# Optimization experiments

Measured on AMD Instinct MI355X. Metric: run time of the kernel, lower is better.

## Reference

```python
import jax, jax.numpy as jnp
import numpy as np

B, T, D, H, W = 256, 512, 64, 128, 256

def _init_linear(key, out_dim, in_dim):
    lim = 1.0 / np.sqrt(in_dim)
    return jax.random.uniform(key, (out_dim, in_dim), jnp.float32, -lim, lim)

def setup_inputs():
    key = jax.random.key(0)
    ks = jax.random.split(key, 12)
    inp = {}
    inp['ts'] = jnp.arange(T, dtype=jnp.float32)
    for n, k in zip(['coeffs_d', 'coeffs_c', 'coeffs_b', 'coeffs_a'], ks[:4]):
        inp[n] = jax.random.normal(k, (B, T - 1, D), jnp.float32) * 0.05
    # initial MLP: D -> W -> W -> H (relu hidden, identity final)
    inp['i_w0'] = _init_linear(ks[4], W, D); inp['i_b0'] = jnp.zeros((W,), jnp.float32)
    inp['i_w1'] = _init_linear(ks[5], W, W); inp['i_b1'] = jnp.zeros((W,), jnp.float32)
    inp['i_w2'] = _init_linear(ks[6], H, W); inp['i_b2'] = jnp.zeros((H,), jnp.float32)
    # func MLP: H -> W -> W -> H*D (softplus hidden, tanh final)
    inp['f_w0'] = _init_linear(ks[7], W, H); inp['f_b0'] = jnp.zeros((W,), jnp.float32)
    inp['f_w1'] = _init_linear(ks[8], W, W); inp['f_b1'] = jnp.zeros((W,), jnp.float32)
    inp['f_w2'] = _init_linear(ks[9], H * D, W); inp['f_b2'] = jnp.zeros((H * D,), jnp.float32)
    # readout linear: H -> 1
    inp['l_w'] = _init_linear(ks[10], 1, H); inp['l_b'] = jnp.zeros((1,), jnp.float32)
    return inp

def reference(ts, coeffs_d, coeffs_c, coeffs_b, coeffs_a,
              i_w0, i_b0, i_w1, i_b1, i_w2, i_b2,
              f_w0, f_b0, f_w1, f_b1, f_w2, f_b2,
              l_w, l_b):
    dt = ts[1] - ts[0]
    # cubic spline value at t=ts[0]: interval 0, frac 0 -> a[0]
    x0 = coeffs_a[:, 0, :]  # [B, D]
    h = jax.nn.relu(x0 @ i_w0.T + i_b0)
    h = jax.nn.relu(h @ i_w1.T + i_b1)
    y0 = h @ i_w2.T + i_b2  # [B, H]

    def step(carry, _):
        t, y = carry
        # cubic spline derivative at t: b + 2c*frac + 3d*frac^2 on interval idx
        idx = jnp.clip(jnp.searchsorted(ts, t, side='right') - 1, 0, T - 2)
        frac = t - ts[idx]
        deriv = coeffs_b[:, idx] + 2.0 * coeffs_c[:, idx] * frac + 3.0 * coeffs_d[:, idx] * (frac * frac)  # [B, D]
        # vector field f(y): [B, H, D]
        g = jax.nn.softplus(y @ f_w0.T + f_b0)
        g = jax.nn.softplus(g @ f_w1.T + f_b1)
        f = jnp.tanh(g @ f_w2.T + f_b2).reshape(B, H, D)
        # Euler step: y1 = y + (f @ dX/dt) * dt
        y1 = y + jnp.einsum('bhd,bd->bh', f, deriv) * dt
        return (t + dt, y1), y1

    _, ys = jax.lax.scan(step, (ts[0], y0), None, length=T)
    # prediction = sigmoid(linear(ys[-1]))[0], per batch element
    return jax.nn.sigmoid(ys[-1] @ l_w.T + l_b)[:, 0]  # [B]
```

## Files before the change

### kernel.cpp

```cpp
#include <hip/hip_runtime.h>
#include <hip/hip_bf16.h>
#include <stdint.h>


#define BB 256
#define DD 64
#define HH 128
#define WW 256
#define HD 8192
#define TSTEPS 512
#define PAD_Y 136
#define PAD_G 264

#define SM_W2   0
#define SM_YB   131072
#define SM_G    140288
#define SM_PBUF 157184
#define SM_TOT  158208

typedef __bf16 bf16x8 __attribute__((ext_vector_type(8)));
typedef __bf16 bf16x4 __attribute__((ext_vector_type(4)));
typedef float f32x4 __attribute__((ext_vector_type(4)));

__device__ __forceinline__ float softplus_f(float x) {
  return (x > 15.f) ? x : __logf(1.f + __expf(x));
}
__device__ __forceinline__ float tanh_f(float x) {
  float e = __expf(2.f * x);
  return 1.f - 2.f / (e + 1.f);
}
__device__ __forceinline__ void publish_y(uint32_t* slot, int idx, float val, uint32_t tag) {
  unsigned short ub = __builtin_bit_cast(unsigned short, (__bf16)val);
  __hip_atomic_store(&slot[idx], (tag << 16) | (uint32_t)ub,
                     __ATOMIC_RELAXED, __HIP_MEMORY_SCOPE_AGENT);
}

__global__ void prep_kernel(const float* __restrict__ w0, const float* __restrict__ w1,
                            const float* __restrict__ w2,
                            __bf16* __restrict__ w0b, __bf16* __restrict__ w1b,
                            __bf16* __restrict__ w2b) {
  int stride = gridDim.x * blockDim.x;
  int i0 = blockIdx.x * blockDim.x + threadIdx.x;
  for (int i = i0; i < WW * HH; i += stride) w0b[i] = (__bf16)w0[i];
  for (int i = i0; i < WW * WW; i += stride) w1b[i] = (__bf16)w1[i];
  for (int i = i0; i < HD * WW; i += stride) w2b[i] = (__bf16)w2[i];
}

__global__ __launch_bounds__(256) void init_kernel(
    const float* __restrict__ ca, const float* __restrict__ iw0, const float* __restrict__ ib0,
    const float* __restrict__ iw1, const float* __restrict__ ib1,
    const float* __restrict__ iw2, const float* __restrict__ ib2,
    float* __restrict__ y0) {
  __shared__ float x0[DD];
  __shared__ float h0[WW];
  __shared__ float h1[WW];
  int b = blockIdx.x, t = threadIdx.x;
  if (t < DD) x0[t] = ca[((size_t)b * 511) * DD + t];
  __syncthreads();
  float a = ib0[t];
  for (int d = 0; d < DD; ++d) a = fmaf(x0[d], iw0[t * DD + d], a);
  h0[t] = fmaxf(a, 0.f);
  __syncthreads();
  a = ib1[t];
  for (int d = 0; d < WW; ++d) a = fmaf(h0[d], iw1[t * WW + d], a);
  h1[t] = fmaxf(a, 0.f);
  __syncthreads();
  if (t < HH) {
    a = ib2[t];
    for (int d = 0; d < WW; ++d) a = fmaf(h1[d], iw2[t * WW + d], a);
    y0[b * HH + t] = a;
  }
}

__global__ __attribute__((amdgpu_flat_work_group_size(512, 512), amdgpu_waves_per_eu(2, 2)))
void step_persist(
    const __bf16* __restrict__ w0b, const __bf16* __restrict__ w1b, const __bf16* __restrict__ w2b,
    const float* __restrict__ fb0, const float* __restrict__ fb1, const float* __restrict__ fb2,
    const float* __restrict__ cbp, const float* __restrict__ ccp, const float* __restrict__ cdp,
    float* __restrict__ yA, uint32_t* __restrict__ pk)
{
  extern __shared__ __align__(16) char smem[];
  __bf16* w2l = (__bf16*)(smem + SM_W2);
  __bf16* yb  = (__bf16*)(smem + SM_YB);
  __bf16* g   = (__bf16*)(smem + SM_G);
  float* pbuf = (float*)(smem + SM_PBUF);

  const int tid = threadIdx.x;
  const int wv = tid >> 6;
  const int l = tid & 63;
  const int l16 = l & 15;
  const int lq = l >> 4;

  const int wid = blockIdx.x;
  const int grp = wid >> 5;
  const int j = wid & 31;
  const int rb = grp * 32;
  const int c0 = j * 256;

  for (int blk = tid; blk < 8192; blk += 512) {
    int kq = blk >> 8, col = blk & 255;
    int kb = kq >> 2, lq2 = kq & 3;
    *(bf16x8*)&w2l[(size_t)blk * 8] =
        *(const bf16x8*)&w2b[(size_t)(c0 + col) * WW + kb * 32 + lq2 * 8];
  }

  f32x4 b0r[2], b1r[2], b2r[2];
  #pragma unroll
  for (int c = 0; c < 2; ++c) {
    b0r[c] = *(const f32x4*)&fb0[wv * 32 + c * 16 + lq * 4];
    b1r[c] = *(const f32x4*)&fb1[wv * 32 + c * 16 + lq * 4];
    b2r[c] = *(const f32x4*)&fb2[c0 + wv * 32 + c * 16 + lq * 4];
  }

  size_t cb2[2];
  #pragma unroll
  for (int bt = 0; bt < 2; ++bt)
    cb2[bt] = ((size_t)(rb + bt * 16 + l16) * 511) * DD + (wv & 1) * 32 + lq * 4;

  const int w2base = lq * 2048 + (wv * 32 + l16) * 8;

  float yreg = 0.f;
  int myidx = 0;
  if (tid < 128) {
    int r = tid & 31, hl = tid >> 5;
    myidx = (rb + r) * HH + (4 * j + hl);
    yreg = yA[myidx];
    publish_y(pk, myidx, yreg, 1u);
  }
  __syncthreads();

  for (int k = 0; k < TSTEPS; ++k) {
    const uint32_t want = (uint32_t)(k + 1);
    const uint32_t* src = pk + (size_t)(k & 1) * (BB * HH);

    bf16x8 w0f[4][2], w1f[8][2];
    #pragma unroll
    for (int c = 0; c < 2; ++c) {
      int col = wv * 32 + c * 16 + l16;
      #pragma unroll
      for (int kb = 0; kb < 4; ++kb)
        w0f[kb][c] = *(const bf16x8*)&w0b[col * HH + kb * 32 + lq * 8];
      #pragma unroll
      for (int kb = 0; kb < 8; ++kb)
        w1f[kb][c] = *(const bf16x8*)&w1b[col * WW + kb * 32 + lq * 8];
    }
    __asm__ __volatile__("" ::: "memory");

    {
      uint32_t v[8];
      int ad[8];
      #pragma unroll
      for (int q = 0; q < 8; ++q) {
        int i = tid + q * 512;
        ad[q] = (rb + (i >> 7)) * HH + (i & (HH - 1));
        v[q] = __hip_atomic_load(&src[ad[q]], __ATOMIC_RELAXED, __HIP_MEMORY_SCOPE_AGENT);
      }
      int spins = 0;
      bool allok;
      do {
        allok = true;
        #pragma unroll
        for (int q = 0; q < 8; ++q) {
          if ((v[q] >> 16) != want) {
            allok = false;
            v[q] = __hip_atomic_load(&src[ad[q]], __ATOMIC_RELAXED, __HIP_MEMORY_SCOPE_AGENT);
          }
        }
        if (!allok) {
          __builtin_amdgcn_s_sleep(1);
          if (++spins > (1 << 20)) break;
        }
      } while (!allok);
      #pragma unroll
      for (int q = 0; q < 8; ++q) {
        int i = tid + q * 512;
        yb[(i >> 7) * PAD_Y + (i & (HH - 1))] =
            __builtin_bit_cast(__bf16, (unsigned short)(v[q] & 0xFFFFu));
      }
    }
    __syncthreads();

    {
      f32x4 acc[2][2] = {};
      #pragma unroll
      for (int kb = 0; kb < 4; ++kb) {
        bf16x8 y0 = *(const bf16x8*)&yb[l16 * PAD_Y + kb * 32 + lq * 8];
        bf16x8 y1 = *(const bf16x8*)&yb[(16 + l16) * PAD_Y + kb * 32 + lq * 8];
        #pragma unroll
        for (int c = 0; c < 2; ++c) {
          acc[c][0] = __builtin_amdgcn_mfma_f32_16x16x32_bf16(w0f[kb][c], y0, acc[c][0], 0, 0, 0);
          acc[c][1] = __builtin_amdgcn_mfma_f32_16x16x32_bf16(w0f[kb][c], y1, acc[c][1], 0, 0, 0);
        }
      }
      #pragma unroll
      for (int c = 0; c < 2; ++c)
        #pragma unroll
        for (int bt = 0; bt < 2; ++bt) {
          bf16x4 o;
          #pragma unroll
          for (int r = 0; r < 4; ++r)
            o[r] = (__bf16)softplus_f(acc[c][bt][r] + b0r[c][r]);
          *(bf16x4*)&g[(bt * 16 + l16) * PAD_G + wv * 32 + c * 16 + lq * 4] = o;
        }
    }
    __syncthreads();

    f32x4 dv_[2][2];
    {
      size_t ko = (size_t)((k <= 510) ? k : 510) * DD;
      #pragma unroll
      for (int bt = 0; bt < 2; ++bt)
        #pragma unroll
        for (int c = 0; c < 2; ++c) {
          size_t off = cb2[bt] + ko + c * 16;
          dv_[bt][c] = *(const f32x4*)&cbp[off];
          if (k == 511) {
            f32x4 cc = *(const f32x4*)&ccp[off];
            f32x4 dd = *(const f32x4*)&cdp[off];
            #pragma unroll
            for (int r = 0; r < 4; ++r)
              dv_[bt][c][r] += 2.f * cc[r] + 3.f * dd[r];
          }
        }
    }

    f32x4 acc1[2][2] = {};
    {
      #pragma unroll
      for (int kb = 0; kb < 8; ++kb) {
        bf16x8 a0 = *(const bf16x8*)&g[l16 * PAD_G + kb * 32 + lq * 8];
        bf16x8 a1 = *(const bf16x8*)&g[(16 + l16) * PAD_G + kb * 32 + lq * 8];
        #pragma unroll
        for (int c = 0; c < 2; ++c) {
          acc1[c][0] = __builtin_amdgcn_mfma_f32_16x16x32_bf16(w1f[kb][c], a0, acc1[c][0], 0, 0, 0);
          acc1[c][1] = __builtin_amdgcn_mfma_f32_16x16x32_bf16(w1f[kb][c], a1, acc1[c][1], 0, 0, 0);
        }
      }
    }
    __syncthreads();

    #pragma unroll
    for (int c = 0; c < 2; ++c)
      #pragma unroll
      for (int bt = 0; bt < 2; ++bt) {
        bf16x4 o;
        #pragma unroll
        for (int r = 0; r < 4; ++r)
          o[r] = (__bf16)softplus_f(acc1[c][bt][r] + b1r[c][r]);
        *(bf16x4*)&g[(bt * 16 + l16) * PAD_G + wv * 32 + c * 16 + lq * 4] = o;
      }
    __syncthreads();

    {
      f32x4 acc[2][2] = {};
      #pragma unroll
      for (int kb = 0; kb < 8; ++kb) {
        bf16x8 a0 = *(const bf16x8*)&g[l16 * PAD_G + kb * 32 + lq * 8];
        bf16x8 a1 = *(const bf16x8*)&g[(16 + l16) * PAD_G + kb * 32 + lq * 8];
        #pragma unroll
        for (int c = 0; c < 2; ++c) {
          bf16x8 wf = *(const bf16x8*)&w2l[w2base + kb * 8192 + c * 128];
          acc[c][0] = __builtin_amdgcn_mfma_f32_16x16x32_bf16(wf, a0, acc[c][0], 0, 0, 0);
          acc[c][1] = __builtin_amdgcn_mfma_f32_16x16x32_bf16(wf, a1, acc[c][1], 0, 0, 0);
        }
      }
      #pragma unroll
      for (int bt = 0; bt < 2; ++bt) {
        float p = 0.f;
        #pragma unroll
        for (int c = 0; c < 2; ++c) {
          #pragma unroll
          for (int r = 0; r < 4; ++r) {
            float f = tanh_f(acc[c][bt][r] + b2r[c][r]);
            p = fmaf(f, dv_[bt][c][r], p);
          }
        }
        p += __shfl_xor(p, 16);
        p += __shfl_xor(p, 32);
        if (l < 16) pbuf[wv * 32 + bt * 16 + l] = p;
      }
    }
    __syncthreads();

    if (tid < 128) {
      int hl = tid >> 5, r = tid & 31;
      yreg += pbuf[(2 * hl) * 32 + r] + pbuf[(2 * hl + 1) * 32 + r];
      publish_y(pk + (size_t)((k + 1) & 1) * (BB * HH), myidx, yreg, (uint32_t)(k + 2));
    }
    __syncthreads();
  }

  if (tid < 128) yA[myidx] = yreg;
}

__global__ __launch_bounds__(256) void final_kernel(const float* __restrict__ y,
                                                    const float* __restrict__ lw,
                                                    const float* __restrict__ lb,
                                                    float* __restrict__ out) {
  int b = threadIdx.x;
  float a = lb[0];
  for (int h = 0; h < HH; ++h) a = fmaf(y[b * HH + h], lw[h], a);
  out[b] = 1.f / (1.f + __expf(-a));
}

extern "C" void kernel_launch(void* const* d_in, const int* in_sizes, int n_in,
                              void* d_out, int out_size, void* d_ws, size_t ws_size,
                              hipStream_t stream) {
  const float* cdp = (const float*)d_in[1];
  const float* ccp = (const float*)d_in[2];
  const float* cbp = (const float*)d_in[3];
  const float* cap = (const float*)d_in[4];
  const float* iw0 = (const float*)d_in[5];
  const float* ib0 = (const float*)d_in[6];
  const float* iw1 = (const float*)d_in[7];
  const float* ib1 = (const float*)d_in[8];
  const float* iw2 = (const float*)d_in[9];
  const float* ib2 = (const float*)d_in[10];
  const float* fw0 = (const float*)d_in[11];
  const float* fb0 = (const float*)d_in[12];
  const float* fw1 = (const float*)d_in[13];
  const float* fb1 = (const float*)d_in[14];
  const float* fw2 = (const float*)d_in[15];
  const float* fb2 = (const float*)d_in[16];
  const float* lw  = (const float*)d_in[17];
  const float* lb  = (const float*)d_in[18];

  char* ws = (char*)d_ws;
  __bf16* w0b = (__bf16*)(ws);
  __bf16* w1b = (__bf16*)(ws + 65536);
  __bf16* w2b = (__bf16*)(ws + 65536 + 131072);
  float* yA = (float*)(ws + 65536 + 131072 + 4194304);
  uint32_t* pk = (uint32_t*)(ws + 65536 + 131072 + 4194304 + 131072);

  hipMemsetAsync(pk, 0, 2 * BB * HH * sizeof(uint32_t), stream);
  prep_kernel<<<512, 256, 0, stream>>>(fw0, fw1, fw2, w0b, w1b, w2b);
  init_kernel<<<BB, 256, 0, stream>>>(cap, iw0, ib0, iw1, ib1, iw2, ib2, yA);
  step_persist<<<256, 512, SM_TOT, stream>>>(w0b, w1b, w2b, fb0, fb1, fb2,
                                             cbp, ccp, cdp, yA, pk);
  final_kernel<<<1, 256, 0, stream>>>(yA, lw, lb, (float*)d_out);

  (void)in_sizes; (void)n_in; (void)out_size; (void)ws_size;
}
```

Baseline: 4.361 ms.

## Split each block's batch tile into two 16-row halves and publish per half

Each persistent block now handles its 32 batch rows as two 16-row sub-tiles, processed one after the other within each time step. Each half waits only for its own 16 rows of y and publishes them as soon as it finishes. The intent is to overlap the grid-wide spin-wait latency of one half with the compute of the other, and to give layer 1 and layer 2 separate shared-memory buffers so one barrier goes away. In exchange, the bf16 weight fragments are reloaded from global memory twice per step, each MFMA pass has half the batch width, and there are more barriers per step.

```diff
diff --git a/kernel.cpp b/kernel.cpp
--- a/kernel.cpp
+++ b/kernel.cpp
@@ -14,9 +14,10 @@
 
 #define SM_W2   0
 #define SM_YB   131072
-#define SM_G    140288
-#define SM_PBUF 157184
-#define SM_TOT  158208
+#define SM_G0   135424
+#define SM_G1   143872
+#define SM_PBUF 152320
+#define SM_TOT  152832
 
 typedef __bf16 bf16x8 __attribute__((ext_vector_type(8)));
 typedef __bf16 bf16x4 __attribute__((ext_vector_type(4)));
@@ -28,6 +29,9 @@
 __device__ __forceinline__ float tanh_f(float x) {
   float e = __expf(2.f * x);
   return 1.f - 2.f / (e + 1.f);
+}
+__device__ __forceinline__ uint32_t aload(const uint32_t* p) {
+  return __hip_atomic_load(p, __ATOMIC_RELAXED, __HIP_MEMORY_SCOPE_AGENT);
 }
 __device__ __forceinline__ void publish_y(uint32_t* slot, int idx, float val, uint32_t tag) {
   unsigned short ub = __builtin_bit_cast(unsigned short, (__bf16)val);
@@ -82,7 +86,8 @@
   extern __shared__ __align__(16) char smem[];
   __bf16* w2l = (__bf16*)(smem + SM_W2);
   __bf16* yb  = (__bf16*)(smem + SM_YB);
-  __bf16* g   = (__bf16*)(smem + SM_G);
+  __bf16* g0s = (__bf16*)(smem + SM_G0);
+  __bf16* g1s = (__bf16*)(smem + SM_G1);
   float* pbuf = (float*)(smem + SM_PBUF);
 
   const int tid = threadIdx.x;
@@ -92,9 +97,9 @@
   const int lq = l >> 4;
 
   const int wid = blockIdx.x;
-  const int grp = wid >> 5;
+  const int p = wid >> 5;
   const int j = wid & 31;
-  const int rb = grp * 32;
+  const int rb0 = p * 32;
   const int c0 = j * 256;
 
   for (int blk = tid; blk < 8192; blk += 512) {
@@ -103,6 +108,7 @@
     *(bf16x8*)&w2l[(size_t)blk * 8] =
         *(const bf16x8*)&w2b[(size_t)(c0 + col) * WW + kb * 32 + lq2 * 8];
   }
+  const int w2base = lq * 2048 + (wv * 32 + l16) * 8;
 
   f32x4 b0r[2], b1r[2], b2r[2];
   #pragma unroll
@@ -114,183 +120,172 @@
 
   size_t cb2[2];
   #pragma unroll
-  for (int bt = 0; bt < 2; ++bt)
-    cb2[bt] = ((size_t)(rb + bt * 16 + l16) * 511) * DD + (wv & 1) * 32 + lq * 4;
-
-  const int w2base = lq * 2048 + (wv * 32 + l16) * 8;
-
-  float yreg = 0.f;
-  int myidx = 0;
-  if (tid < 128) {
-    int r = tid & 31, hl = tid >> 5;
-    myidx = (rb + r) * HH + (4 * j + hl);
-    yreg = yA[myidx];
-    publish_y(pk, myidx, yreg, 1u);
+  for (int s = 0; s < 2; ++s)
+    cb2[s] = ((size_t)(rb0 + 16 * s + l16) * 511) * DD + (wv & 1) * 32 + lq * 4;
+
+  float yreg[2] = {0.f, 0.f};
+  int myidx[2] = {0, 0};
+  if (tid < 64) {
+    int r = tid & 15, hl = tid >> 4;
+    #pragma unroll
+    for (int s = 0; s < 2; ++s) {
+      myidx[s] = (rb0 + 16 * s + r) * HH + (4 * j + hl);
+      yreg[s] = yA[myidx[s]];
+      publish_y(pk, myidx[s], yreg[s], 1u);
+    }
   }
   __syncthreads();
 
   for (int k = 0; k < TSTEPS; ++k) {
     const uint32_t want = (uint32_t)(k + 1);
     const uint32_t* src = pk + (size_t)(k & 1) * (BB * HH);
-
-    bf16x8 w0f[4][2], w1f[8][2];
+    uint32_t* dst = pk + (size_t)((k + 1) & 1) * (BB * HH);
+
     #pragma unroll
-    for (int c = 0; c < 2; ++c) {
-      int col = wv * 32 + c * 16 + l16;
+    for (int s = 0; s < 2; ++s) {
+      const int rbs = rb0 + 16 * s;
+
+      bf16x8 w0f[4][2], w1f[8][2];
       #pragma unroll
-      for (int kb = 0; kb < 4; ++kb)
-        w0f[kb][c] = *(const bf16x8*)&w0b[col * HH + kb * 32 + lq * 8];
-      #pragma unroll
-      for (int kb = 0; kb < 8; ++kb)
-        w1f[kb][c] = *(const bf16x8*)&w1b[col * WW + kb * 32 + lq * 8];
-    }
-    __asm__ __volatile__("" ::: "memory");
-
-    {
-      uint32_t v[8];
-      int ad[8];
-      #pragma unroll
-      for (int q = 0; q < 8; ++q) {
-        int i = tid + q * 512;
-        ad[q] = (rb + (i >> 7)) * HH + (i & (HH - 1));
-        v[q] = __hip_atomic_load(&src[ad[q]], __ATOMIC_RELAXED, __HIP_MEMORY_SCOPE_AGENT);
-      }
-      int spins = 0;
-      bool allok;
-      do {
-        allok = true;
-        #pragma unroll
-        for (int q = 0; q < 8; ++q) {
-          if ((v[q] >> 16) != want) {
-            allok = false;
-            v[q] = __hip_atomic_load(&src[ad[q]], __ATOMIC_RELAXED, __HIP_MEMORY_SCOPE_AGENT);
-          }
-        }
-        if (!allok) {
-          __builtin_amdgcn_s_sleep(1);
-          if (++spins > (1 << 20)) break;
-        }
-      } while (!allok);
-      #pragma unroll
-      for (int q = 0; q < 8; ++q) {
-        int i = tid + q * 512;
-        yb[(i >> 7) * PAD_Y + (i & (HH - 1))] =
-            __builtin_bit_cast(__bf16, (unsigned short)(v[q] & 0xFFFFu));
-      }
-    }
-    __syncthreads();
-
-    {
-      f32x4 acc[2][2] = {};
-      #pragma unroll
-      for (int kb = 0; kb < 4; ++kb) {
-        bf16x8 y0 = *(const bf16x8*)&yb[l16 * PAD_Y + kb * 32 + lq * 8];
-        bf16x8 y1 = *(const bf16x8*)&yb[(16 + l16) * PAD_Y + kb * 32 + lq * 8];
+      for (int c = 0; c < 2; ++c) {
+        int col = wv * 32 + c * 16 + l16;
+        #pragma unroll
+        for (int kb = 0; kb < 4; ++kb)
+          w0f[kb][c] = *(const bf16x8*)&w0b[col * HH + kb * 32 + lq * 8];
+        #pragma unroll
+        for (int kb = 0; kb < 8; ++kb)
+          w1f[kb][c] = *(const bf16x8*)&w1b[col * WW + kb * 32 + lq * 8];
+      }
+      __asm__ __volatile__("" ::: "memory");
+
+      {
+        uint32_t v[4];
+        int ad[4];
+        #pragma unroll
+        for (int q = 0; q < 4; ++q) {
+          int i = tid + q * 512;
+          ad[q] = (rbs + (i >> 7)) * HH + (i & 127);
+          v[q] = aload(&src[ad[q]]);
+        }
+        int spins = 0;
+        bool allok;
+        do {
+          allok = true;
+          #pragma unroll
+          for (int q = 0; q < 4; ++q) {
+            if ((v[q] >> 16) != want) {
+              allok = false;
+              v[q] = aload(&src[ad[q]]);
+            }
+          }
+          if (!allok) {
+            __builtin_amdgcn_s_sleep(1);
+            if (++spins > (1 << 20)) break;
+          }
+        } while (!allok);
+        #pragma unroll
+        for (int q = 0; q < 4; ++q) {
+          int i = tid + q * 512;
+          yb[(i >> 7) * PAD_Y + (i & 127)] =
+              __builtin_bit_cast(__bf16, (unsigned short)(v[q] & 0xFFFFu));
+        }
+      }
+
+      f32x4 dvv[2];
+      {
+        size_t ko = (size_t)((k <= 510) ? k : 510) * DD;
         #pragma unroll
         for (int c = 0; c < 2; ++c) {
-          acc[c][0] = __builtin_amdgcn_mfma_f32_16x16x32_bf16(w0f[kb][c], y0, acc[c][0], 0, 0, 0);
-          acc[c][1] = __builtin_amdgcn_mfma_f32_16x16x32_bf16(w0f[kb][c], y1, acc[c][1], 0, 0, 0);
-        }
-      }
-      #pragma unroll
-      for (int c = 0; c < 2; ++c)
-        #pragma unroll
-        for (int bt = 0; bt < 2; ++bt) {
-          bf16x4 o;
-          #pragma unroll
-          for (int r = 0; r < 4; ++r)
-            o[r] = (__bf16)softplus_f(acc[c][bt][r] + b0r[c][r]);
-          *(bf16x4*)&g[(bt * 16 + l16) * PAD_G + wv * 32 + c * 16 + lq * 4] = o;
-        }
-    }
-    __syncthreads();
-
-    f32x4 dv_[2][2];
-    {
-      size_t ko = (size_t)((k <= 510) ? k : 510) * DD;
-      #pragma unroll
-      for (int bt = 0; bt < 2; ++bt)
-        #pragma unroll
-        for (int c = 0; c < 2; ++c) {
-          size_t off = cb2[bt] + ko + c * 16;
-          dv_[bt][c] = *(const f32x4*)&cbp[off];
+          size_t off = cb2[s] + ko + c * 16;
+          dvv[c] = *(const f32x4*)&cbp[off];
           if (k == 511) {
             f32x4 cc = *(const f32x4*)&ccp[off];
             f32x4 dd = *(const f32x4*)&cdp[off];
             #pragma unroll
             for (int r = 0; r < 4; ++r)
-              dv_[bt][c][r] += 2.f * cc[r] + 3.f * dd[r];
-          }
-        }
+              dvv[c][r] += 2.f * cc[r] + 3.f * dd[r];
+          }
+        }
+      }
+      __syncthreads();
+
+      {
+        f32x4 acc[2] = {};
+        #pragma unroll
+        for (int kb = 0; kb < 4; ++kb) {
+          bf16x8 y0 = *(const bf16x8*)&yb[l16 * PAD_Y + kb * 32 + lq * 8];
+          #pragma unroll
+          for (int c = 0; c < 2; ++c)
+            acc[c] = __builtin_amdgcn_mfma_f32_16x16x32_bf16(w0f[kb][c], y0, acc[c], 0, 0, 0);
+        }
+        #pragma unroll
+        for (int c = 0; c < 2; ++c) {
+          bf16x4 o;
+          #pragma unroll
+          for (int r = 0; r < 4; ++r)
+            o[r] = (__bf16)softplus_f(acc[c][r] + b0r[c][r]);
+          *(bf16x4*)&g0s[l16 * PAD_G + wv * 32 + c * 16 + lq * 4] = o;
+        }
+      }
+      __syncthreads();
+
+      {
+        f32x4 acc[2] = {};
+        #pragma unroll
+        for (int kb = 0; kb < 8; ++kb) {
+          bf16x8 a0 = *(const bf16x8*)&g0s[l16 * PAD_G + kb * 32 + lq * 8];
+          #pragma unroll
+          for (int c = 0; c < 2; ++c)
+            acc[c] = __builtin_amdgcn_mfma_f32_16x16x32_bf16(w1f[kb][c], a0, acc[c], 0, 0, 0);
+        }
+        #pragma unroll
+        for (int c = 0; c < 2; ++c) {
+          bf16x4 o;
+          #pragma unroll
+          for (int r = 0; r < 4; ++r)
+            o[r] = (__bf16)softplus_f(acc[c][r] + b1r[c][r]);
+          *(bf16x4*)&g1s[l16 * PAD_G + wv * 32 + c * 16 + lq * 4] = o;
+        }
+      }
+      __syncthreads();
+
+      {
+        f32x4 acc[2] = {};
+        #pragma unroll
+        for (int kb = 0; kb < 8; ++kb) {
+          bf16x8 a0 = *(const bf16x8*)&g1s[l16 * PAD_G + kb * 32 + lq * 8];
+          #pragma unroll
+          for (int c = 0; c < 2; ++c) {
+            bf16x8 wf = *(const bf16x8*)&w2l[w2base + kb * 8192 + c * 128];
+            acc[c] = __builtin_amdgcn_mfma_f32_16x16x32_bf16(wf, a0, acc[c], 0, 0, 0);
+          }
+        }
+        float pp = 0.f;
+        #pragma unroll
+        for (int c = 0; c < 2; ++c)
+          #pragma unroll
+          for (int r = 0; r < 4; ++r) {
+            float f = tanh_f(acc[c][r] + b2r[c][r]);
+            pp = fmaf(f, dvv[c][r], pp);
+          }
+        pp += __shfl_xor(pp, 16);
+        pp += __shfl_xor(pp, 32);
+        if (l < 16) pbuf[wv * 16 + l] = pp;
+      }
+      __syncthreads();
+
+      if (tid < 64) {
+        int r = tid & 15, hl = tid >> 4;
+        yreg[s] += pbuf[(2 * hl) * 16 + r] + pbuf[(2 * hl + 1) * 16 + r];
+        publish_y(dst, myidx[s], yreg[s], (uint32_t)(k + 2));
+      }
     }
-
-    f32x4 acc1[2][2] = {};
-    {
-      #pragma unroll
-      for (int kb = 0; kb < 8; ++kb) {
-        bf16x8 a0 = *(const bf16x8*)&g[l16 * PAD_G + kb * 32 + lq * 8];
-        bf16x8 a1 = *(const bf16x8*)&g[(16 + l16) * PAD_G + kb * 32 + lq * 8];
-        #pragma unroll
-        for (int c = 0; c < 2; ++c) {
-          acc1[c][0] = __builtin_amdgcn_mfma_f32_16x16x32_bf16(w1f[kb][c], a0, acc1[c][0], 0, 0, 0);
-          acc1[c][1] = __builtin_amdgcn_mfma_f32_16x16x32_bf16(w1f[kb][c], a1, acc1[c][1], 0, 0, 0);
-        }
-      }
-    }
-    __syncthreads();
-
-    #pragma unroll
-    for (int c = 0; c < 2; ++c)
-      #pragma unroll
-      for (int bt = 0; bt < 2; ++bt) {
-        bf16x4 o;
-        #pragma unroll
-        for (int r = 0; r < 4; ++r)
-          o[r] = (__bf16)softplus_f(acc1[c][bt][r] + b1r[c][r]);
-        *(bf16x4*)&g[(bt * 16 + l16) * PAD_G + wv * 32 + c * 16 + lq * 4] = o;
-      }
-    __syncthreads();
-
-    {
-      f32x4 acc[2][2] = {};
-      #pragma unroll
-      for (int kb = 0; kb < 8; ++kb) {
-        bf16x8 a0 = *(const bf16x8*)&g[l16 * PAD_G + kb * 32 + lq * 8];
-        bf16x8 a1 = *(const bf16x8*)&g[(16 + l16) * PAD_G + kb * 32 + lq * 8];
-        #pragma unroll
-        for (int c = 0; c < 2; ++c) {
-          bf16x8 wf = *(const bf16x8*)&w2l[w2base + kb * 8192 + c * 128];
-          acc[c][0] = __builtin_amdgcn_mfma_f32_16x16x32_bf16(wf, a0, acc[c][0], 0, 0, 0);
-          acc[c][1] = __builtin_amdgcn_mfma_f32_16x16x32_bf16(wf, a1, acc[c][1], 0, 0, 0);
-        }
-      }
-      #pragma unroll
-      for (int bt = 0; bt < 2; ++bt) {
-        float p = 0.f;
-        #pragma unroll
-        for (int c = 0; c < 2; ++c) {
-          #pragma unroll
-          for (int r = 0; r < 4; ++r) {
-            float f = tanh_f(acc[c][bt][r] + b2r[c][r]);
-            p = fmaf(f, dv_[bt][c][r], p);
-          }
-        }
-        p += __shfl_xor(p, 16);
-        p += __shfl_xor(p, 32);
-        if (l < 16) pbuf[wv * 32 + bt * 16 + l] = p;
-      }
-    }
-    __syncthreads();
-
-    if (tid < 128) {
-      int hl = tid >> 5, r = tid & 31;
-      yreg += pbuf[(2 * hl) * 32 + r] + pbuf[(2 * hl + 1) * 32 + r];
-      publish_y(pk + (size_t)((k + 1) & 1) * (BB * HH), myidx, yreg, (uint32_t)(k + 2));
-    }
-    __syncthreads();
-  }
-
-  if (tid < 128) yA[myidx] = yreg;
+  }
+
+  if (tid < 64) {
+    yA[myidx[0]] = yreg[0];
+    yA[myidx[1]] = yreg[1];
+  }
 }
 
 __global__ __launch_bounds__(256) void final_kernel(const float* __restrict__ y,
```

New measurement: 7.025 ms. 1.61x slower.
